# Performance work log

Measured on AMD Instinct MI355X. Metric: run time of the kernel, lower is better.

The kernel has to match this reference:

```python
import jax, jax.numpy as jnp
import numpy as np

SEQ_LEN = 2049  # conf.SEQ_LEN; sequence axis of inputs is SEQ_LEN - 1
BATCH = 1024
N_FEAT = 11

# Static lookup table of type masks (rows 0..7 per the if/elif ladder; row 8 = all-False 'else').
# Rows 4..6 are placeholders: they are replaced by the dynamic prefix-count branch.
_TYPE_TABLE = np.zeros((9, 8), dtype=bool)
_TYPE_TABLE[0] = [0, 1, 0, 0, 0, 0, 0, 0]
_TYPE_TABLE[1] = [0, 1, 1, 0, 0, 0, 0, 0]
_TYPE_TABLE[2] = [0, 0, 0, 0, 1, 0, 0, 0]
_TYPE_TABLE[3] = [0, 0, 0, 1, 1, 1, 1, 1]
_TYPE_TABLE[7] = [0, 0, 0, 0, 0, 0, 0, 1]

_MASK_NO_TIMESIGN = np.array([0, 0, 0, 0, 0, 1, 0, 0], dtype=bool)  # time_sign_occurrences == 0
_MASK_NO_TEMPO    = np.array([0, 0, 0, 0, 0, 0, 1, 0], dtype=bool)  # tempo_occurrences == 0
_MASK_FULL        = np.array([0, 0, 0, 1, 1, 1, 1, 1], dtype=bool)  # both present -> same as type 3


def setup_inputs() -> dict:
    key = jax.random.key(0)
    inputs = jax.random.randint(key, (BATCH, SEQ_LEN - 1, N_FEAT), 0, 8, dtype=jnp.int32)
    return {"inputs": inputs}


def reference(inputs) -> jnp.ndarray:
    gt = inputs[:, :, 0]                       # [B, L] token types, L = SEQ_LEN - 1
    B, L = gt.shape

    # Base masks from the static per-type table ('else' -> row 8, all False).
    table = jnp.asarray(_TYPE_TABLE)
    base = table[jnp.clip(gt, 0, 8)]           # [B, L, 8]

    # Prefix counts: for token i, count types over positions j with j <= i + 1 (inclusive).
    is5 = (gt == 5).astype(jnp.int32)
    is6 = (gt == 6).astype(jnp.int32)
    c5 = jnp.cumsum(is5, axis=1)               # inclusive cumsum
    c6 = jnp.cumsum(is6, axis=1)
    idx = jnp.minimum(jnp.arange(L) + 1, L - 1)  # position i looks at prefix up to min(i+1, L-1)
    cnt5 = c5[:, idx]                           # [B, L] time_sign occurrences
    cnt6 = c6[:, idx]                           # [B, L] tempo occurrences

    # Dynamic branch for token types 4..6.
    no_ts = (cnt5 == 0)[..., None]              # [B, L, 1]
    no_tp = (cnt6 == 0)[..., None]
    dyn = jnp.where(no_ts, jnp.asarray(_MASK_NO_TIMESIGN),
                    jnp.where(no_tp, jnp.asarray(_MASK_NO_TEMPO), jnp.asarray(_MASK_FULL)))  # [B, L, 8]

    cond456 = ((gt >= 4) & (gt <= 6))[..., None]
    masks = jnp.where(cond456, dyn, base)       # [B, L, 8] bool
    return masks
```

## Files before the change

kernel.cpp:

```cpp
#include <hip/hip_runtime.h>


#define SEQ_L 2048
#define NF 11
#define BLOCK 512
#define ROW_INT4 (SEQ_L * NF / 4)
#define PASSES (ROW_INT4 / BLOCK)
#define OUT_INT4 (SEQ_L * 8 / 4)
#define OPASS (OUT_INT4 / BLOCK)

__global__ __launch_bounds__(BLOCK)
void mask_type_prob_kernel(const int* __restrict__ in, int* __restrict__ out) {
    __shared__ int s_gt[SEQ_L];
    __shared__ int s_first5;
    __shared__ int s_first6;

    const int b   = blockIdx.x;
    const int tid = threadIdx.x;

    if (tid == 0) { s_first5 = 0x7FFFFFFF; s_first6 = 0x7FFFFFFF; }
    __syncthreads();

    const int4* rowv = (const int4*)(in + (size_t)b * SEQ_L * NF);

    int4 v[PASSES];
    #pragma unroll
    for (int p = 0; p < PASSES; ++p) {
        v[p] = rowv[tid + p * BLOCK];
    }

    int f5 = 0x7FFFFFFF, f6 = 0x7FFFFFFF;
    #pragma unroll
    for (int p = 0; p < PASSES; ++p) {
        const int i4 = tid + p * BLOCK;
        const int j  = i4 * 4;
        const int mi  = (j + 10) / 11;
        const int pos = mi * 11 - j;
        if (pos < 4) {
            const int gv = (pos == 0) ? v[p].x : (pos == 1) ? v[p].y
                         : (pos == 2) ? v[p].z : v[p].w;
            s_gt[mi] = gv;
            if (gv == 5) f5 = min(f5, mi);
            if (gv == 6) f6 = min(f6, mi);
        }
    }

    #pragma unroll
    for (int off = 32; off >= 1; off >>= 1) {
        f5 = min(f5, __shfl_xor(f5, off, 64));
        f6 = min(f6, __shfl_xor(f6, off, 64));
    }
    if ((tid & 63) == 0) {
        if (f5 != 0x7FFFFFFF) atomicMin(&s_first5, f5);
        if (f6 != 0x7FFFFFFF) atomicMin(&s_first6, f6);
    }
    __syncthreads();

    const int first5 = s_first5;
    const int first6 = s_first6;

    const unsigned long long pack = 0x80000000F8100602ULL;

    int4* orowv = (int4*)(out + (size_t)b * SEQ_L * 8);

    #pragma unroll
    for (int k = 0; k < OPASS; ++k) {
        const int c    = tid + k * BLOCK;
        const int t    = c >> 1;
        const int half = c & 1;
        const int gv   = s_gt[t];
        unsigned m;
        if (gv >= 4 && gv <= 6) {
            const int idx = (t + 1 < SEQ_L - 1) ? (t + 1) : (SEQ_L - 1);
            m = (first5 > idx) ? 0x20u : ((first6 > idx) ? 0x40u : 0xF8u);
        } else {
            int gc = gv < 0 ? 0 : (gv > 8 ? 8 : gv);
            m = (gc >= 8) ? 0u : (unsigned)((pack >> (gc * 8)) & 0xFFu);
        }
        const unsigned nib = half ? (m >> 4) : m;
        int4 w;
        w.x = (int)((nib >> 0) & 1u);
        w.y = (int)((nib >> 1) & 1u);
        w.z = (int)((nib >> 2) & 1u);
        w.w = (int)((nib >> 3) & 1u);
        orowv[c] = w;
    }
}

extern "C" void kernel_launch(void* const* d_in, const int* in_sizes, int n_in,
                              void* d_out, int out_size, void* d_ws, size_t ws_size,
                              hipStream_t stream) {
    const int* in = (const int*)d_in[0];
    int* out = (int*)d_out;
    const int batch = in_sizes[0] / (SEQ_L * NF);
    mask_type_prob_kernel<<<batch, BLOCK, 0, stream>>>(in, out);
}
```

Before: 153.6 us.

## Split fused mask kernel into reduce and emit kernels via workspace

Splits the single per-row kernel into two. The first reads the inputs, writes the extracted token types to a global workspace and records the first positions of types 5 and 6. The second launches four times as many smaller blocks to emit the output masks. This aims to raise parallelism in the write-heavy emit phase, at the cost of an extra launch and a global round trip for the token types (8 MB written and read back).

```diff
diff --git a/kernel.cpp b/kernel.cpp
--- a/kernel.cpp
+++ b/kernel.cpp
@@ -3,78 +3,76 @@
 
 #define SEQ_L 2048
 #define NF 11
-#define BLOCK 512
-#define ROW_INT4 (SEQ_L * NF / 4)
-#define PASSES (ROW_INT4 / BLOCK)
-#define OUT_INT4 (SEQ_L * 8 / 4)
-#define OPASS (OUT_INT4 / BLOCK)
 
-__global__ __launch_bounds__(BLOCK)
-void mask_type_prob_kernel(const int* __restrict__ in, int* __restrict__ out) {
-    __shared__ int s_gt[SEQ_L];
-    __shared__ int s_first5;
-    __shared__ int s_first6;
-
+__global__ __launch_bounds__(512)
+void mask_reduce_kernel(const int* __restrict__ in, int* __restrict__ gt_out,
+                        unsigned* __restrict__ first5, unsigned* __restrict__ first6) {
+    __shared__ unsigned s_f5, s_f6;
     const int b   = blockIdx.x;
     const int tid = threadIdx.x;
-
-    if (tid == 0) { s_first5 = 0x7FFFFFFF; s_first6 = 0x7FFFFFFF; }
+    if (tid == 0) { s_f5 = 0xFFFFFFFFu; s_f6 = 0xFFFFFFFFu; }
     __syncthreads();
 
     const int4* rowv = (const int4*)(in + (size_t)b * SEQ_L * NF);
+    int4 v[11];
+    #pragma unroll
+    for (int p = 0; p < 11; ++p) v[p] = rowv[tid + p * 512];
 
-    int4 v[PASSES];
+    unsigned f5 = 0xFFFFFFFFu, f6 = 0xFFFFFFFFu;
+    int* grow = gt_out + b * SEQ_L;
     #pragma unroll
-    for (int p = 0; p < PASSES; ++p) {
-        v[p] = rowv[tid + p * BLOCK];
-    }
-
-    int f5 = 0x7FFFFFFF, f6 = 0x7FFFFFFF;
-    #pragma unroll
-    for (int p = 0; p < PASSES; ++p) {
-        const int i4 = tid + p * BLOCK;
+    for (int p = 0; p < 11; ++p) {
+        const int i4 = tid + p * 512;
         const int j  = i4 * 4;
         const int mi  = (j + 10) / 11;
         const int pos = mi * 11 - j;
         if (pos < 4) {
             const int gv = (pos == 0) ? v[p].x : (pos == 1) ? v[p].y
                          : (pos == 2) ? v[p].z : v[p].w;
-            s_gt[mi] = gv;
-            if (gv == 5) f5 = min(f5, mi);
-            if (gv == 6) f6 = min(f6, mi);
+            grow[mi] = gv;
+            if (gv == 5) f5 = min(f5, (unsigned)mi);
+            if (gv == 6) f6 = min(f6, (unsigned)mi);
         }
     }
-
     #pragma unroll
     for (int off = 32; off >= 1; off >>= 1) {
-        f5 = min(f5, __shfl_xor(f5, off, 64));
-        f6 = min(f6, __shfl_xor(f6, off, 64));
+        f5 = min(f5, (unsigned)__shfl_xor((int)f5, off, 64));
+        f6 = min(f6, (unsigned)__shfl_xor((int)f6, off, 64));
     }
     if ((tid & 63) == 0) {
-        if (f5 != 0x7FFFFFFF) atomicMin(&s_first5, f5);
-        if (f6 != 0x7FFFFFFF) atomicMin(&s_first6, f6);
+        if (f5 != 0xFFFFFFFFu) atomicMin(&s_f5, f5);
+        if (f6 != 0xFFFFFFFFu) atomicMin(&s_f6, f6);
     }
     __syncthreads();
+    if (tid == 0) { first5[b] = s_f5; first6[b] = s_f6; }
+}
 
-    const int first5 = s_first5;
-    const int first6 = s_first6;
+__global__ __launch_bounds__(256)
+void mask_emit_kernel(const int* __restrict__ gt, const unsigned* __restrict__ first5,
+                      const unsigned* __restrict__ first6, int* __restrict__ out) {
+    const int bid = blockIdx.x;
+    const int row = bid >> 2;
+    const int tid = threadIdx.x;
+    const unsigned f5 = first5[row];
+    const unsigned f6 = first6[row];
+    const int* grow = gt + row * SEQ_L;
+    int4* orow = (int4*)(out + (size_t)row * SEQ_L * 8);
+    const int cbase = (bid & 3) * 1024;
 
     const unsigned long long pack = 0x80000000F8100602ULL;
 
-    int4* orowv = (int4*)(out + (size_t)b * SEQ_L * 8);
-
     #pragma unroll
-    for (int k = 0; k < OPASS; ++k) {
-        const int c    = tid + k * BLOCK;
-        const int t    = c >> 1;
-        const int half = c & 1;
-        const int gv   = s_gt[t];
+    for (int k = 0; k < 4; ++k) {
+        const int cr   = cbase + k * 256 + tid;
+        const int t    = cr >> 1;
+        const int half = cr & 1;
+        const int gv   = grow[t];
         unsigned m;
         if (gv >= 4 && gv <= 6) {
-            const int idx = (t + 1 < SEQ_L - 1) ? (t + 1) : (SEQ_L - 1);
-            m = (first5 > idx) ? 0x20u : ((first6 > idx) ? 0x40u : 0xF8u);
+            const unsigned idx = (unsigned)((t + 1 < SEQ_L - 1) ? (t + 1) : (SEQ_L - 1));
+            m = (f5 > idx) ? 0x20u : ((f6 > idx) ? 0x40u : 0xF8u);
         } else {
-            int gc = gv < 0 ? 0 : (gv > 8 ? 8 : gv);
+            const int gc = gv < 0 ? 0 : (gv > 8 ? 8 : gv);
             m = (gc >= 8) ? 0u : (unsigned)((pack >> (gc * 8)) & 0xFFu);
         }
         const unsigned nib = half ? (m >> 4) : m;
@@ -83,7 +81,7 @@
         w.y = (int)((nib >> 1) & 1u);
         w.z = (int)((nib >> 2) & 1u);
         w.w = (int)((nib >> 3) & 1u);
-        orowv[c] = w;
+        orow[cr] = w;
     }
 }
 
@@ -93,5 +91,11 @@
     const int* in = (const int*)d_in[0];
     int* out = (int*)d_out;
     const int batch = in_sizes[0] / (SEQ_L * NF);
-    mask_type_prob_kernel<<<batch, BLOCK, 0, stream>>>(in, out);
+
+    unsigned* first5 = (unsigned*)d_ws;
+    unsigned* first6 = first5 + batch;
+    int* gt = (int*)(first6 + batch);
+
+    mask_reduce_kernel<<<batch, 512, 0, stream>>>(in, gt, first5, first6);
+    mask_emit_kernel<<<batch * 4, 256, 0, stream>>>(gt, first5, first6, out);
 }
```

New measurement: 156.1 us. Within noise of the previous version (+1.6%).
